# Kernel optimization log

Hardware: AMD Instinct MI355X
Metric: run time of the kernel (lower is better)

The kernel has to match this reference:

```python
import jax, jax.numpy as jnp
import numpy as np

B, S, D = 4, 4096, 256


def setup_inputs() -> dict:
    key = jax.random.key(0)
    ks = jax.random.split(key, 7)
    s = 1.0 / np.sqrt(D)
    return {
        "x": jax.random.normal(ks[0], (B, S, D), dtype=jnp.float32),
        "Wq": jax.random.uniform(ks[1], (D, D), jnp.float32, -s, s),
        "bq": jax.random.uniform(ks[2], (D,), jnp.float32, -s, s),
        "Wk": jax.random.uniform(ks[3], (D, D), jnp.float32, -s, s),
        "bk": jax.random.uniform(ks[4], (D,), jnp.float32, -s, s),
        "Wv": jax.random.uniform(ks[5], (D, D), jnp.float32, -s, s),
        "bv": jax.random.uniform(ks[6], (D,), jnp.float32, -s, s),
    }


def reference(x, Wq, bq, Wk, bk, Wv, bv):
    # nn.Linear: y = x @ W.T + b
    Q = jnp.einsum("bsd,ed->bse", x, Wq) + bq
    K = jnp.einsum("bsd,ed->bse", x, Wk) + bk
    V = jnp.einsum("bsd,ed->bse", x, Wv) + bv
    dk = Q.shape[-1]
    scores = jnp.einsum("bqd,bkd->bqk", Q, K) / jnp.sqrt(jnp.float32(dk))
    # NOTE: original applies softmax over dim=1 (the query axis), not -1.
    attn = jax.nn.softmax(scores, axis=1)
    out = jnp.einsum("bqk,bkd->bqd", attn, V)
    return out
```

## Files before the change

### kernel.cpp

```cpp
#include <hip/hip_runtime.h>

typedef short bf16x8 __attribute__((ext_vector_type(8)));
typedef float f32x4 __attribute__((ext_vector_type(4)));
typedef unsigned short u16;

#define S_LEN 4096
#define D_DIM 256
#define NROW  16384

__device__ __forceinline__ u16 f2bf(float f) {
    union { float f; unsigned u; } v; v.f = f;
    unsigned r = v.u + 0x7FFFu + ((v.u >> 16) & 1u);
    return (u16)(r >> 16);
}

__device__ __forceinline__ size_t fr_qk(int t, int kk) {
    return (size_t)t * 4096 + kk * 512;
}
__device__ __forceinline__ size_t fr_v(int p, int dt, int kk2) {
    return (size_t)p * 16384 + (dt * 2 + kk2) * 512;
}

__device__ __forceinline__ void gll16(const u16* g, u16* l) {
    __builtin_amdgcn_global_load_lds(
        (const __attribute__((address_space(1))) unsigned int*)g,
        (__attribute__((address_space(3))) unsigned int*)l, 16, 0, 0);
}

__global__ __launch_bounds__(256) void wconv(
    const float* __restrict__ Wq, const float* __restrict__ Wk,
    const float* __restrict__ Wv, u16* __restrict__ Wf)
{
    int i = blockIdx.x * 256 + threadIdx.x;
    int m = i >> 13;
    int idx = i & 8191;
    int ocol = idx >> 5;
    int d0 = (idx & 31) * 8;
    const float* s = (m == 0 ? Wq : (m == 1 ? Wk : Wv)) + ocol * 256 + d0;
    float4 v0 = *reinterpret_cast<const float4*>(s);
    float4 v1 = *reinterpret_cast<const float4*>(s + 4);
    union { ushort4 h[2]; int4 q; } t;
    t.h[0] = make_ushort4(f2bf(v0.x), f2bf(v0.y), f2bf(v0.z), f2bf(v0.w));
    t.h[1] = make_ushort4(f2bf(v1.x), f2bf(v1.y), f2bf(v1.z), f2bf(v1.w));
    size_t off = (size_t)m * 65536 + fr_qk(ocol >> 4, d0 >> 5)
               + ((d0 >> 3) & 3) * 128 + (ocol & 15) * 8;
    *reinterpret_cast<int4*>(Wf + off) = t.q;
}

__global__ __launch_bounds__(256) void qkv_proj(
    const float* __restrict__ x, const u16* __restrict__ Wf,
    const float* __restrict__ bq, const float* __restrict__ bk,
    const float* __restrict__ bv,
    u16* __restrict__ Qf, u16* __restrict__ Kf, u16* __restrict__ Vf)
{
    __shared__ u16 xs[32][264];
    const int tid = threadIdx.x;
    const int r0 = blockIdx.x * 32;

    #pragma unroll
    for (int i = 0; i < 8; ++i) {
        int c = i * 256 + tid;
        int row = c >> 6, c4 = c & 63;
        float4 v = reinterpret_cast<const float4*>(x + (size_t)(r0 + row) * D_DIM)[c4];
        *reinterpret_cast<ushort4*>(&xs[row][c4 * 4]) =
            make_ushort4(f2bf(v.x), f2bf(v.y), f2bf(v.z), f2bf(v.w));
    }
    __syncthreads();

    const int w = tid >> 6, l = tid & 63, lr = l & 15, lg = l >> 4;
    const int c0 = w * 64;

    bf16x8 a[2][8];
    #pragma unroll
    for (int qs = 0; qs < 2; ++qs)
        #pragma unroll
        for (int kk = 0; kk < 8; ++kk)
            a[qs][kk] = *reinterpret_cast<const bf16x8*>(&xs[qs * 16 + lr][kk * 32 + lg * 8]);

    const float* Bs[3] = {bq, bk, bv};

    #pragma unroll
    for (int m = 0; m < 3; ++m) {
        const u16* Wm = Wf + (size_t)m * 65536;
        f32x4 acc[2][4] = {};
        #pragma unroll
        for (int kk = 0; kk < 8; ++kk) {
            #pragma unroll
            for (int cf = 0; cf < 4; ++cf) {
                bf16x8 wfr = *reinterpret_cast<const bf16x8*>(
                    Wm + fr_qk(w * 4 + cf, kk) + l * 8);
                acc[0][cf] = __builtin_amdgcn_mfma_f32_16x16x32_bf16(a[0][kk], wfr, acc[0][cf], 0, 0, 0);
                acc[1][cf] = __builtin_amdgcn_mfma_f32_16x16x32_bf16(a[1][kk], wfr, acc[1][cf], 0, 0, 0);
            }
        }
        if (m < 2) {
            u16* outp = (m == 0) ? Qf : Kf;
            int t = r0 >> 4;
            #pragma unroll
            for (int qs = 0; qs < 2; ++qs) {
                #pragma unroll
                for (int cf = 0; cf < 4; ++cf) {
                    int col = c0 + cf * 16 + lr;
                    float bias = Bs[m][col];
                    size_t base = fr_qk(t + qs, col >> 5) + ((col >> 3) & 3) * 128 + (col & 7);
                    #pragma unroll
                    for (int r = 0; r < 4; ++r)
                        outp[base + (lg * 4 + r) * 8] = f2bf(acc[qs][cf][r] + bias);
                }
            }
        } else {
            int p  = (r0 >> 12) * 64 + ((r0 & 4095) >> 6);
            int kb = r0 & 63;
            #pragma unroll
            for (int qs = 0; qs < 2; ++qs) {
                #pragma unroll
                for (int cf = 0; cf < 4; ++cf) {
                    int d = c0 + cf * 16 + lr;
                    float bias = bv[d];
                    #pragma unroll
                    for (int r = 0; r < 4; ++r) {
                        int key = kb + qs * 16 + lg * 4 + r;
                        size_t off = fr_v(p, d >> 4, key >> 5)
                                   + ((key >> 3) & 3) * 128 + (d & 15) * 8 + (key & 7);
                        Vf[off] = f2bf(acc[qs][cf][r] + bias);
                    }
                }
            }
        }
    }
}

__global__ __launch_bounds__(256, 2) void col_denom(
    const u16* __restrict__ Qf, const u16* __restrict__ Kf, float* __restrict__ Zp)
{
    __shared__ __align__(16) u16 Qls[2][8192];
    const int tid = threadIdx.x, blk = blockIdx.x;
    const int xcd = blk & 7, sub = blk >> 3;
    const int b  = xcd >> 1;
    const int qq = ((xcd & 1) << 1) | (sub & 1);
    const int ktile = sub >> 1;
    const int w = tid >> 6, l = tid & 63, lr = l & 15, lg = l >> 4;
    const int k0 = ktile * 128;

    bf16x8 kreg[2][8];
    #pragma unroll
    for (int ks = 0; ks < 2; ++ks) {
        const int tk = b * 256 + (k0 >> 4) + w * 2 + ks;
        #pragma unroll
        for (int kk = 0; kk < 8; ++kk)
            kreg[ks][kk] = *reinterpret_cast<const bf16x8*>(Kf + fr_qk(tk, kk) + l * 8);
    }

    #define STAGE_Q(qt_, nb_) do { \
        const u16* g_ = Qf + ((size_t)(b * 256 + (qt_) * 2)) * 4096 + (w * 4) * 512 + l * 8; \
        u16* d_ = &Qls[nb_][(w * 4) * 512]; \
        _Pragma("unroll") \
        for (int f_ = 0; f_ < 4; ++f_) gll16(g_ + f_ * 512, d_ + f_ * 512); \
    } while (0)

    const int qt0 = qq * 32;
    STAGE_Q(qt0, 0);
    __syncthreads();

    float Z[2][4] = {};
    const float SC = 0.0625f;

    for (int it = 0; it < 32; ++it) {
        const int cur = it & 1;
        if (it < 31) STAGE_Q(qt0 + it + 1, cur ^ 1);

        f32x4 acc[2][2] = {};
        #pragma unroll
        for (int kk = 0; kk < 8; ++kk) {
            #pragma unroll
            for (int qf = 0; qf < 2; ++qf) {
                bf16x8 qfr = *reinterpret_cast<const bf16x8*>(
                    &Qls[cur][(qf * 8 + kk) * 512 + l * 8]);
                acc[0][qf] = __builtin_amdgcn_mfma_f32_16x16x32_bf16(kreg[0][kk], qfr, acc[0][qf], 0, 0, 0);
                acc[1][qf] = __builtin_amdgcn_mfma_f32_16x16x32_bf16(kreg[1][kk], qfr, acc[1][qf], 0, 0, 0);
            }
        }
        #pragma unroll
        for (int ks = 0; ks < 2; ++ks)
            #pragma unroll
            for (int qf = 0; qf < 2; ++qf)
                #pragma unroll
                for (int r = 0; r < 4; ++r)
                    Z[ks][r] += __expf(acc[ks][qf][r] * SC);
        __syncthreads();
    }

    #pragma unroll
    for (int ks = 0; ks < 2; ++ks) {
        #pragma unroll
        for (int r = 0; r < 4; ++r) {
            float z = Z[ks][r];
            z += __shfl_xor(z, 1);
            z += __shfl_xor(z, 2);
            z += __shfl_xor(z, 4);
            z += __shfl_xor(z, 8);
            if (lr == 0)
                Zp[qq * NROW + b * S_LEN + k0 + w * 32 + ks * 16 + lg * 4 + r] = z;
        }
    }
    #undef STAGE_Q
}

__global__ __launch_bounds__(256) void zlog(
    const float* __restrict__ Zp, float* __restrict__ LZ)
{
    int i = blockIdx.x * 256 + threadIdx.x;
    LZ[i] = logf(((Zp[i] + Zp[NROW + i]) + Zp[2 * NROW + i]) + Zp[3 * NROW + i]);
}

__global__ __launch_bounds__(256, 2) void attn_out(
    const u16* __restrict__ Qf, const u16* __restrict__ Kf, const u16* __restrict__ Vf,
    const float* __restrict__ LZ, float* __restrict__ out)
{
    __shared__ __align__(16) u16 Kls[2][8192];
    __shared__ __align__(16) u16 Vls[2][8192];
    __shared__ __align__(16) u16 ps[4][1280];

    const int tid = threadIdx.x, blk = blockIdx.x;
    const int xcd = blk & 7, sub = blk >> 3;
    const int b  = xcd >> 1;
    const int kq = ((xcd & 1) << 1) | (sub & 1);
    const int qtile = sub >> 1;
    const int w = tid >> 6, l = tid & 63, lr = l & 15, lg = l >> 4;
    const int q0 = qtile * 128 + w * 32;
    const int base_tk = b * 256;

    bf16x8 qreg[2][8];
    #pragma unroll
    for (int qs = 0; qs < 2; ++qs) {
        const int tq = base_tk + ((q0 + qs * 16) >> 4);
        #pragma unroll
        for (int kk = 0; kk < 8; ++kk)
            qreg[qs][kk] = *reinterpret_cast<const bf16x8*>(Qf + fr_qk(tq, kk) + l * 8);
    }

    #define STAGE_KV(kt_, nb_) do { \
        if (w < 2) { \
            const u16* g_ = Kf + ((size_t)(base_tk + (kt_) * 2)) * 4096 + (w * 8) * 512 + l * 8; \
            u16* d_ = &Kls[nb_][(w * 8) * 512]; \
            _Pragma("unroll") \
            for (int f_ = 0; f_ < 8; ++f_) gll16(g_ + f_ * 512, d_ + f_ * 512); \
        } else { \
            const size_t vb_ = ((size_t)(b * 64 + ((kt_) >> 1))) * 16384 + ((kt_) & 1) * 512; \
            const int dt0_ = (w - 2) * 8; \
            _Pragma("unroll") \
            for (int f_ = 0; f_ < 8; ++f_) \
                gll16(Vf + vb_ + (size_t)(dt0_ + f_) * 1024 + l * 8, &Vls[nb_][(dt0_ + f_) * 512]); \
        } \
    } while (0)

    const int kt0 = kq * 32;
    STAGE_KV(kt0, 0);
    __syncthreads();

    f32x4 oacc[2][16] = {};
    const float SC = 0.0625f;

    for (int it = 0; it < 32; ++it) {
        const int kt = kt0 + it;
        const int cur = it & 1;
        if (it < 31) STAGE_KV(kt + 1, cur ^ 1);

        #pragma unroll
        for (int cf = 0; cf < 2; ++cf) {
            float Lv = LZ[b * S_LEN + kt * 32 + cf * 16 + lr];
            f32x4 sacc[2] = {};
            #pragma unroll
            for (int kk = 0; kk < 8; ++kk) {
                bf16x8 kfr = *reinterpret_cast<const bf16x8*>(
                    &Kls[cur][(cf * 8 + kk) * 512 + l * 8]);
                sacc[0] = __builtin_amdgcn_mfma_f32_16x16x32_bf16(qreg[0][kk], kfr, sacc[0], 0, 0, 0);
                sacc[1] = __builtin_amdgcn_mfma_f32_16x16x32_bf16(qreg[1][kk], kfr, sacc[1], 0, 0, 0);
            }
            #pragma unroll
            for (int qs = 0; qs < 2; ++qs) {
                #pragma unroll
                for (int r = 0; r < 4; ++r) {
                    float p = __expf(fmaf(sacc[qs][r], SC, -Lv));
                    ps[w][(qs * 16 + lg * 4 + r) * 40 + cf * 16 + lr] = f2bf(p);
                }
            }
        }
        bf16x8 af0 = *reinterpret_cast<const bf16x8*>(&ps[w][lr * 40 + lg * 8]);
        bf16x8 af1 = *reinterpret_cast<const bf16x8*>(&ps[w][(16 + lr) * 40 + lg * 8]);
        #pragma unroll
        for (int dt = 0; dt < 16; ++dt) {
            bf16x8 vfr = *reinterpret_cast<const bf16x8*>(&Vls[cur][dt * 512 + l * 8]);
            oacc[0][dt] = __builtin_amdgcn_mfma_f32_16x16x32_bf16(af0, vfr, oacc[0][dt], 0, 0, 0);
            oacc[1][dt] = __builtin_amdgcn_mfma_f32_16x16x32_bf16(af1, vfr, oacc[1][dt], 0, 0, 0);
        }
        __syncthreads();
    }

    #pragma unroll
    for (int qs = 0; qs < 2; ++qs) {
        #pragma unroll
        for (int dt = 0; dt < 16; ++dt) {
            #pragma unroll
            for (int r = 0; r < 4; ++r) {
                int row = q0 + qs * 16 + lg * 4 + r;
                unsafeAtomicAdd(&out[((size_t)(b * S_LEN + row)) * D_DIM + dt * 16 + lr],
                                oacc[qs][dt][r]);
            }
        }
    }
    #undef STAGE_KV
}

extern "C" void kernel_launch(void* const* d_in, const int* in_sizes, int n_in,
                              void* d_out, int out_size, void* d_ws, size_t ws_size,
                              hipStream_t stream) {
    const float* x  = (const float*)d_in[0];
    const float* Wq = (const float*)d_in[1];
    const float* bq = (const float*)d_in[2];
    const float* Wk = (const float*)d_in[3];
    const float* bk = (const float*)d_in[4];
    const float* Wv = (const float*)d_in[5];
    const float* bv = (const float*)d_in[6];
    float* out = (float*)d_out;

    u16* Qf = (u16*)d_ws;
    u16* Kf = Qf + (size_t)NROW * D_DIM;
    u16* Vf = Kf + (size_t)NROW * D_DIM;
    u16* Wf = Vf + (size_t)NROW * D_DIM;
    float* Zp = (float*)(Wf + 196608);
    float* LZ = Zp + 4 * NROW;

    hipMemsetAsync(out, 0, (size_t)NROW * D_DIM * sizeof(float), stream);

    wconv<<<96, 256, 0, stream>>>(Wq, Wk, Wv, Wf);
    qkv_proj<<<NROW / 32, 256, 0, stream>>>(x, Wf, bq, bk, bv, Qf, Kf, Vf);
    col_denom<<<512, 256, 0, stream>>>(Qf, Kf, Zp);
    zlog<<<NROW / 256, 256, 0, stream>>>(Zp, LZ);
    attn_out<<<512, 256, 0, stream>>>(Qf, Kf, Vf, LZ, out);
}
```

Measured before the change: 186.0 us.

## Deepen attn_out K/V prefetch to 4-stage ring with 512-thread blocks

Restructures attn_out to use 8 waves per block, each block covering 256 query rows, with a 4-slot LDS ring for K and V tiles prefetched three iterations ahead. Explicit vmcnt waits plus raw barriers replace __syncthreads, and s_setprio raises priority around the MFMA sections. The aim is to hide global-to-LDS load latency and cut per-iteration barrier stalls. LDS use rises to roughly 150 KB, which allows only one block per CU and relies on the manual waitcnt accounting being exact.

```diff
diff --git a/kernel.cpp b/kernel.cpp
--- a/kernel.cpp
+++ b/kernel.cpp
@@ -26,6 +26,10 @@
         (const __attribute__((address_space(1))) unsigned int*)g,
         (__attribute__((address_space(3))) unsigned int*)l, 16, 0, 0);
 }
+
+#define WAITV8 asm volatile("s_waitcnt vmcnt(8)" ::: "memory")
+#define WAITV0 asm volatile("s_waitcnt vmcnt(0)" ::: "memory")
+#define MEMFENCE asm volatile("" ::: "memory")
 
 __global__ __launch_bounds__(256) void wconv(
     const float* __restrict__ Wq, const float* __restrict__ Wk,
@@ -213,13 +217,13 @@
     LZ[i] = logf(((Zp[i] + Zp[NROW + i]) + Zp[2 * NROW + i]) + Zp[3 * NROW + i]);
 }
 
-__global__ __launch_bounds__(256, 2) void attn_out(
+__global__ __launch_bounds__(512, 1) void attn_out(
     const u16* __restrict__ Qf, const u16* __restrict__ Kf, const u16* __restrict__ Vf,
     const float* __restrict__ LZ, float* __restrict__ out)
 {
-    __shared__ __align__(16) u16 Kls[2][8192];
-    __shared__ __align__(16) u16 Vls[2][8192];
-    __shared__ __align__(16) u16 ps[4][1280];
+    __shared__ __align__(16) u16 Kls[4][8192];
+    __shared__ __align__(16) u16 Vls[4][8192];
+    __shared__ __align__(16) u16 ps[8][1280];
 
     const int tid = threadIdx.x, blk = blockIdx.x;
     const int xcd = blk & 7, sub = blk >> 3;
@@ -227,8 +231,9 @@
     const int kq = ((xcd & 1) << 1) | (sub & 1);
     const int qtile = sub >> 1;
     const int w = tid >> 6, l = tid & 63, lr = l & 15, lg = l >> 4;
-    const int q0 = qtile * 128 + w * 32;
+    const int q0 = qtile * 256 + w * 32;
     const int base_tk = b * 256;
+    const int kt0 = kq * 32;
 
     bf16x8 qreg[2][8];
     #pragma unroll
@@ -239,62 +244,86 @@
             qreg[qs][kk] = *reinterpret_cast<const bf16x8*>(Qf + fr_qk(tq, kk) + l * 8);
     }
 
-    #define STAGE_KV(kt_, nb_) do { \
-        if (w < 2) { \
-            const u16* g_ = Kf + ((size_t)(base_tk + (kt_) * 2)) * 4096 + (w * 8) * 512 + l * 8; \
-            u16* d_ = &Kls[nb_][(w * 8) * 512]; \
-            _Pragma("unroll") \
-            for (int f_ = 0; f_ < 8; ++f_) gll16(g_ + f_ * 512, d_ + f_ * 512); \
+    #define STAGE(kt_, nb_) do { \
+        if (w < 4) { \
+            const u16* g_ = Kf + ((size_t)(base_tk + (kt0 + (kt_)) * 2)) * 4096 + (w * 4) * 512 + l * 8; \
+            u16* d_ = &Kls[nb_][(w * 4) * 512]; \
+            _Pragma("unroll") \
+            for (int f_ = 0; f_ < 4; ++f_) gll16(g_ + f_ * 512, d_ + f_ * 512); \
         } else { \
-            const size_t vb_ = ((size_t)(b * 64 + ((kt_) >> 1))) * 16384 + ((kt_) & 1) * 512; \
-            const int dt0_ = (w - 2) * 8; \
-            _Pragma("unroll") \
-            for (int f_ = 0; f_ < 8; ++f_) \
+            const int kta_ = kt0 + (kt_); \
+            const size_t vb_ = ((size_t)(b * 64 + (kta_ >> 1))) * 16384 + (kta_ & 1) * 512; \
+            const int dt0_ = (w - 4) * 4; \
+            _Pragma("unroll") \
+            for (int f_ = 0; f_ < 4; ++f_) \
                 gll16(Vf + vb_ + (size_t)(dt0_ + f_) * 1024 + l * 8, &Vls[nb_][(dt0_ + f_) * 512]); \
         } \
     } while (0)
 
-    const int kt0 = kq * 32;
-    STAGE_KV(kt0, 0);
-    __syncthreads();
+    #define BODY(kt_) do { \
+        const int cur_ = (kt_) & 3; \
+        const int ktabs_ = kt0 + (kt_); \
+        _Pragma("unroll") \
+        for (int cf = 0; cf < 2; ++cf) { \
+            float Lv = LZ[b * S_LEN + ktabs_ * 32 + cf * 16 + lr]; \
+            f32x4 sacc[2] = {}; \
+            __builtin_amdgcn_s_setprio(1); \
+            _Pragma("unroll") \
+            for (int kk = 0; kk < 8; ++kk) { \
+                bf16x8 kfr = *reinterpret_cast<const bf16x8*>( \
+                    &Kls[cur_][(cf * 8 + kk) * 512 + l * 8]); \
+                sacc[0] = __builtin_amdgcn_mfma_f32_16x16x32_bf16(qreg[0][kk], kfr, sacc[0], 0, 0, 0); \
+                sacc[1] = __builtin_amdgcn_mfma_f32_16x16x32_bf16(qreg[1][kk], kfr, sacc[1], 0, 0, 0); \
+            } \
+            __builtin_amdgcn_s_setprio(0); \
+            _Pragma("unroll") \
+            for (int qs = 0; qs < 2; ++qs) \
+                _Pragma("unroll") \
+                for (int r = 0; r < 4; ++r) { \
+                    float p = __expf(fmaf(sacc[qs][r], SC, -Lv)); \
+                    ps[w][(qs * 16 + lg * 4 + r) * 40 + cf * 16 + lr] = f2bf(p); \
+                } \
+        } \
+        { \
+            bf16x8 af0 = *reinterpret_cast<const bf16x8*>(&ps[w][lr * 40 + lg * 8]); \
+            bf16x8 af1 = *reinterpret_cast<const bf16x8*>(&ps[w][(16 + lr) * 40 + lg * 8]); \
+            __builtin_amdgcn_s_setprio(1); \
+            _Pragma("unroll") \
+            for (int dt = 0; dt < 16; ++dt) { \
+                bf16x8 vfr = *reinterpret_cast<const bf16x8*>(&Vls[cur_][dt * 512 + l * 8]); \
+                oacc[0][dt] = __builtin_amdgcn_mfma_f32_16x16x32_bf16(af0, vfr, oacc[0][dt], 0, 0, 0); \
+                oacc[1][dt] = __builtin_amdgcn_mfma_f32_16x16x32_bf16(af1, vfr, oacc[1][dt], 0, 0, 0); \
+            } \
+            __builtin_amdgcn_s_setprio(0); \
+        } \
+    } while (0)
 
     f32x4 oacc[2][16] = {};
     const float SC = 0.0625f;
 
-    for (int it = 0; it < 32; ++it) {
-        const int kt = kt0 + it;
-        const int cur = it & 1;
-        if (it < 31) STAGE_KV(kt + 1, cur ^ 1);
-
-        #pragma unroll
-        for (int cf = 0; cf < 2; ++cf) {
-            float Lv = LZ[b * S_LEN + kt * 32 + cf * 16 + lr];
-            f32x4 sacc[2] = {};
-            #pragma unroll
-            for (int kk = 0; kk < 8; ++kk) {
-                bf16x8 kfr = *reinterpret_cast<const bf16x8*>(
-                    &Kls[cur][(cf * 8 + kk) * 512 + l * 8]);
-                sacc[0] = __builtin_amdgcn_mfma_f32_16x16x32_bf16(qreg[0][kk], kfr, sacc[0], 0, 0, 0);
-                sacc[1] = __builtin_amdgcn_mfma_f32_16x16x32_bf16(qreg[1][kk], kfr, sacc[1], 0, 0, 0);
-            }
-            #pragma unroll
-            for (int qs = 0; qs < 2; ++qs) {
-                #pragma unroll
-                for (int r = 0; r < 4; ++r) {
-                    float p = __expf(fmaf(sacc[qs][r], SC, -Lv));
-                    ps[w][(qs * 16 + lg * 4 + r) * 40 + cf * 16 + lr] = f2bf(p);
-                }
-            }
-        }
-        bf16x8 af0 = *reinterpret_cast<const bf16x8*>(&ps[w][lr * 40 + lg * 8]);
-        bf16x8 af1 = *reinterpret_cast<const bf16x8*>(&ps[w][(16 + lr) * 40 + lg * 8]);
-        #pragma unroll
-        for (int dt = 0; dt < 16; ++dt) {
-            bf16x8 vfr = *reinterpret_cast<const bf16x8*>(&Vls[cur][dt * 512 + l * 8]);
-            oacc[0][dt] = __builtin_amdgcn_mfma_f32_16x16x32_bf16(af0, vfr, oacc[0][dt], 0, 0, 0);
-            oacc[1][dt] = __builtin_amdgcn_mfma_f32_16x16x32_bf16(af1, vfr, oacc[1][dt], 0, 0, 0);
-        }
-        __syncthreads();
+    STAGE(0, 0);
+    STAGE(1, 1);
+    STAGE(2, 2);
+    WAITV8;
+    __builtin_amdgcn_s_barrier();
+    MEMFENCE;
+
+    #pragma unroll 1
+    for (int kt = 0; kt < 29; ++kt) {
+        STAGE(kt + 3, (kt + 3) & 3);
+        BODY(kt);
+        WAITV8;
+        __builtin_amdgcn_s_barrier();
+        MEMFENCE;
+    }
+    #pragma unroll 1
+    for (int kt = 29; kt < 32; ++kt) {
+        BODY(kt);
+        if (kt < 31) {
+            WAITV0;
+            __builtin_amdgcn_s_barrier();
+            MEMFENCE;
+        }
     }
 
     #pragma unroll
@@ -309,7 +338,8 @@
             }
         }
     }
-    #undef STAGE_KV
+    #undef STAGE
+    #undef BODY
 }
 
 extern "C" void kernel_launch(void* const* d_in, const int* in_sizes, int n_in,
@@ -337,5 +367,5 @@
     qkv_proj<<<NROW / 32, 256, 0, stream>>>(x, Wf, bq, bk, bv, Qf, Kf, Vf);
     col_denom<<<512, 256, 0, stream>>>(Qf, Kf, Zp);
     zlog<<<NROW / 256, 256, 0, stream>>>(Zp, LZ);
-    attn_out<<<512, 256, 0, stream>>>(Qf, Kf, Vf, LZ, out);
-}
+    attn_out<<<256, 512, 0, stream>>>(Qf, Kf, Vf, LZ, out);
+}
```

Result: no change. 187.7 us (+0.9%).
